# Optimization experiments

Hardware: AMD Instinct MI355X
Metric: run time of the kernel (lower is better)

Reference implementation:

```python
import jax, jax.numpy as jnp
import numpy as np
import math

IN_FEATURES = 1024
OUT_FEATURES = 1024
GRID_SIZE = 5
SPLINE_ORDER = 3
BATCH = 4096
K = GRID_SIZE + 2 * SPLINE_ORDER  # 11 basis functions per feature


def make_grid():
    h = (1.0 - (-1.0)) / GRID_SIZE
    xx = np.arange(-SPLINE_ORDER, GRID_SIZE + SPLINE_ORDER + 1, dtype=np.float32) * h + (-1.0)
    return jnp.asarray(np.broadcast_to(xx, (IN_FEATURES, xx.shape[0])).copy())  # (in, K+1)


def setup_inputs() -> dict:
    key = jax.random.key(0)
    k1, k2, k3, k4 = jax.random.split(key, 4)
    x = jax.random.normal(k1, (BATCH, IN_FEATURES), dtype=jnp.float32)
    base_weight = jax.random.normal(k2, (OUT_FEATURES, IN_FEATURES), dtype=jnp.float32) * 0.02
    spline_weight = jax.random.normal(k3, (OUT_FEATURES, IN_FEATURES, K), dtype=jnp.float32) * 0.02
    spline_scaler = jax.random.normal(k4, (OUT_FEATURES, IN_FEATURES), dtype=jnp.float32) * 0.1
    return {"x": x, "base_weight": base_weight, "spline_weight": spline_weight,
            "spline_scaler": spline_scaler, "grid": make_grid()}


def trig_basis(x, grid):
    # x: (B, in) ; grid: (in, K+1) -> basis: (B, in, K)
    a = grid[:, :-1]                      # (in, K)
    b = grid[:, 1:]                       # (in, K)
    interval = jnp.maximum(b - a, 1e-8)
    xe = x[:, :, None]                    # (B, in, 1)
    inside = ((xe >= a) & (xe < b)).astype(x.dtype)
    trig = jnp.sin(jnp.pi * (xe - a) / interval)
    return inside * trig


def reference(x, base_weight, spline_weight, spline_scaler, grid):
    # base branch: SiLU(x) @ base_weight^T
    enm = jax.nn.silu(x) @ base_weight.T                     # (B, out)
    # spline branch: fused basis expansion + GEMM
    basis = trig_basis(x, grid)                              # (B, in, K)
    sw = spline_weight * spline_scaler[:, :, None]           # (out, in, K)
    snm = jnp.einsum('bik,oik->bo', basis, sw)               # (B, out)
    return enm + snm
```

## Files before the change

### kernel.cpp

```cpp
#include <hip/hip_runtime.h>
#include <hip/hip_bf16.h>

#define BATCH  4096
#define INF    1024
#define OUTF   1024
#define KSPL   11
#define KSPB   11264
#define SW_SCALE 1016.0f

using bf16    = __hip_bfloat16;
using short8  = __attribute__((ext_vector_type(8))) short;
using ushort8 = __attribute__((ext_vector_type(8))) unsigned short;
using f32x4   = __attribute__((ext_vector_type(4))) float;
using i32x4   = __attribute__((ext_vector_type(4))) int;
typedef unsigned long long u64;

__device__ __forceinline__ unsigned short f2bf(float f){
  union { float f; unsigned u; } a; a.f = f;
  return (unsigned short)((a.u + 0x7FFFu + ((a.u >> 16) & 1u)) >> 16);
}

__device__ __forceinline__ void llds16(const void* g, const void* l){
  __builtin_amdgcn_global_load_lds(
      (const __attribute__((address_space(1))) unsigned int*)g,
      (__attribute__((address_space(3))) unsigned int*)l, 16, 0, 0);
}

__device__ __forceinline__ void bar(){
  asm volatile("" ::: "memory");
  __builtin_amdgcn_s_barrier();
  asm volatile("" ::: "memory");
}

__device__ __forceinline__ f32x4 mfma16(short8 a, short8 b, f32x4 c){
  return __builtin_amdgcn_mfma_f32_16x16x32_bf16(a, b, c, 0, 0, 0);
}
__device__ __forceinline__ i32x4 mfma_i8(i32x4 a, i32x4 b, i32x4 c){
  return __builtin_amdgcn_mfma_i32_16x16x64_i8(a, b, c, 0, 0, 0);
}

__device__ __forceinline__ int swz(int L){ return L ^ (((L>>7)&7)<<4); }

__global__ __launch_bounds__(256) void prep(const float* __restrict__ x,
                                            const float* __restrict__ bw,
                                            const float* __restrict__ sw,
                                            const float* __restrict__ sc,
                                            bf16* __restrict__ A_sil,
                                            char* __restrict__ A_spl,
                                            bf16* __restrict__ W_b,
                                            char* __restrict__ W_s){
  const int t = threadIdx.x;
  if (blockIdx.x < 2048){
    const int gid = blockIdx.x * 256 + t;
    const int b  = gid >> 7;
    const int i0 = (gid & 127) * 8;
    const float* xr = x + (size_t)b * INF + i0;
    f32x4 p0 = *(const f32x4*)xr;
    f32x4 p1 = *(const f32x4*)(xr + 4);
    float v[8];
    #pragma unroll
    for (int j = 0; j < 4; ++j){ v[j] = p0[j]; v[4+j] = p1[j]; }
    ushort8 sl;
    int c[8], q[8];
    #pragma unroll
    for (int j = 0; j < 8; ++j){
      float xx = v[j];
      sl[j] = f2bf(xx / (1.0f + __expf(-xx)));
      float tt = (xx + 1.0f) * 2.5f;
      float fl = floorf(tt);
      c[j] = (int)fl + 3;
      q[j] = (int)rintf(__sinf(3.14159265358979f * (tt - fl)) * 127.0f);
    }
    *(ushort8*)(A_sil + (size_t)b*INF + i0) = sl;
    char* ar = A_spl + (size_t)b * KSPB + i0;
    #pragma unroll
    for (int k = 0; k < KSPL; ++k){
      u64 up = 0;
      #pragma unroll
      for (int j = 0; j < 8; ++j){
        unsigned char byte = (c[j] == k) ? (unsigned char)q[j] : (unsigned char)0;
        up |= ((u64)byte) << (8*j);
      }
      *(u64*)(ar + k*INF) = up;
    }
  } else {
    const int gid = (blockIdx.x - 2048) * 256 + t;
    const int o  = gid >> 7;
    const int i0 = (gid & 127) * 8;
    float buf[88];
    const float* sp = sw + ((size_t)o*INF + i0) * KSPL;
    #pragma unroll
    for (int qd = 0; qd < 22; ++qd)
      ((f32x4*)buf)[qd] = ((const f32x4*)sp)[qd];
    f32x4 c0 = *(const f32x4*)(sc + (size_t)o*INF + i0);
    f32x4 c1 = *(const f32x4*)(sc + (size_t)o*INF + i0 + 4);
    float scv[8];
    #pragma unroll
    for (int j = 0; j < 4; ++j){ scv[j] = c0[j]; scv[4+j] = c1[j]; }
    {
      const float* br = bw + (size_t)o*INF + i0;
      f32x4 v0 = *(const f32x4*)br;
      f32x4 v1 = *(const f32x4*)(br + 4);
      ushort8 u;
      #pragma unroll
      for (int j = 0; j < 4; ++j){ u[j] = f2bf(v0[j]); u[4+j] = f2bf(v1[j]); }
      *(ushort8*)(W_b + (size_t)o*INF + i0) = u;
    }
    char* wr = W_s + (size_t)o * KSPB + i0;
    #pragma unroll
    for (int k = 0; k < KSPL; ++k){
      u64 up = 0;
      #pragma unroll
      for (int j = 0; j < 8; ++j){
        float vv = buf[j*KSPL + k] * scv[j] * SW_SCALE;
        vv = fminf(fmaxf(vv, -127.0f), 127.0f);
        int qq = (int)rintf(vv);
        up |= ((u64)(unsigned char)(signed char)qq) << (8*j);
      }
      *(u64*)(wr + k*INF) = up;
    }
  }
}

template<int NS>
__global__ __launch_bounds__(512, 2) void gemm_i8k(const char* __restrict__ A,
                                                   const char* __restrict__ W,
                                                   short* __restrict__ Cp){
  constexpr int KSPLIT_B = KSPB / NS;
  constexpr int NG       = KSPLIT_B / 64;
  __shared__ __align__(16) char smem[131072];

  const int bid = blockIdx.x;
  const int xcd = bid & 7, local = bid >> 3;
  const int split = xcd >> 1;
  const int mt    = (xcd & 1) * 8 + (local >> 2);
  const int nt    = local & 3;
  const int bm = mt*256, bn = nt*256;

  const int t    = threadIdx.x;
  const int lane = t & 63, w = t >> 6;
  const int wr = w >> 2, wc = w & 3;
  const int r15 = lane & 15, hi = lane >> 4;

  int offA[8], offB[4];
  #pragma unroll
  for (int m = 0; m < 8; ++m){
    int L = (wr*128 + m*16 + r15)*64 + hi*16;
    offA[m] = swz(L);
  }
  #pragma unroll
  for (int n = 0; n < 4; ++n){
    int L = (wc*64 + n*16 + r15)*64 + hi*16;
    offB[n] = 16384 + swz(L);
  }

  const char* gA[2]; const char* gB[2];
  int ldsA[2], ldsB[2];
  #pragma unroll
  for (int j = 0; j < 2; ++j){
    int P = (t + j*512)*16;
    int L = swz(P);
    int row = L >> 6, inner = L & 63;
    gA[j] = A + (size_t)(bm + row)*KSPB + split*KSPLIT_B + inner;
    gB[j] = W + (size_t)(bn + row)*KSPB + split*KSPLIT_B + inner;
    ldsA[j] = j*8192 + w*1024;
    ldsB[j] = 16384 + j*8192 + w*1024;
  }

  #define STAGE(buf, tile) do{ \
    llds16(gA[0] + (tile)*64, smem + (buf)*32768 + ldsA[0]); \
    llds16(gA[1] + (tile)*64, smem + (buf)*32768 + ldsA[1]); \
    llds16(gB[0] + (tile)*64, smem + (buf)*32768 + ldsB[0]); \
    llds16(gB[1] + (tile)*64, smem + (buf)*32768 + ldsB[1]); }while(0)

  i32x4 acc[8][4] = {};
  i32x4 afA[4], afB[4], bfA[4], bfB[4];

  STAGE(0,0);
  STAGE(1,1);
  asm volatile("s_waitcnt vmcnt(4)" ::: "memory");
  bar();
  #pragma unroll
  for (int n = 0; n < 4; ++n) bfA[n] = *(const i32x4*)(smem + offB[n]);
  #pragma unroll
  for (int m = 0; m < 4; ++m) afA[m] = *(const i32x4*)(smem + offA[m]);

  #define BODY(tt, curA, curB, nxtA, nxtB) do{                                \
    const char* bp_ = smem + ((tt)&3)*32768;                                  \
    const char* bq_ = smem + (((tt)+1)&3)*32768;                              \
    if ((tt) + 2 < NG){                                                       \
      STAGE(((tt)+2)&3, (tt)+2);                                              \
      asm volatile("s_waitcnt vmcnt(4)" ::: "memory");                        \
    } else {                                                                  \
      asm volatile("s_waitcnt vmcnt(0)" ::: "memory");                        \
    }                                                                         \
    bar();                                                                    \
    i32x4 ag_[4];                                                             \
    __builtin_amdgcn_s_setprio(1);                                            \
    _Pragma("unroll")                                                         \
    for (int m = 0; m < 4; ++m){                                              \
      ag_[m] = *(const i32x4*)(bp_ + offA[4+m]);                              \
      _Pragma("unroll")                                                       \
      for (int n = 0; n < 4; ++n)                                             \
        acc[m][n] = mfma_i8(curA[m], curB[n], acc[m][n]);                     \
    }                                                                         \
    _Pragma("unroll")                                                         \
    for (int m = 0; m < 4; ++m){                                              \
      if ((tt) + 1 < NG){                                                     \
        nxtA[m] = *(const i32x4*)(bq_ + offA[m]);                             \
        nxtB[m] = *(const i32x4*)(bq_ + offB[m]);                             \
      }                                                                       \
      _Pragma("unroll")                                                       \
      for (int n = 0; n < 4; ++n)                                             \
        acc[4+m][n] = mfma_i8(ag_[m], curB[n], acc[4+m][n]);                  \
    }                                                                         \
    __builtin_amdgcn_s_setprio(0);                                            \
  }while(0)

  #pragma unroll 1
  for (int s = 0; s < NG/2; ++s){
    BODY(2*s,   afA, bfA, afB, bfB);
    BODY(2*s+1, afB, bfB, afA, bfA);
  }
  #undef BODY
  #undef STAGE

  short* outp = Cp + (size_t)split * (BATCH*OUTF);
  #pragma unroll
  for (int m = 0; m < 8; ++m){
    const int r0 = bm + wr*128 + m*16 + hi*4;
    #pragma unroll
    for (int n = 0; n < 4; ++n){
      const int cc = bn + wc*64 + n*16 + r15;
      #pragma unroll
      for (int j = 0; j < 4; ++j){
        int v = acc[m][n][j];
        v = (v >  32767) ?  32767 : v;
        v = (v < -32768) ? -32768 : v;
        outp[(size_t)(r0 + j) * OUTF + cc] = (short)v;
      }
    }
  }
}

__global__ __launch_bounds__(512, 2) void gemm_e(const bf16* __restrict__ A,
                                                 const bf16* __restrict__ W,
                                                 const short* __restrict__ Cp,
                                                 float* __restrict__ out){
  constexpr int NG = 32;
  __shared__ __align__(16) char smem[49152];

  const int bid = blockIdx.x;
  const int fin = (bid & 7) * 32 + (bid >> 3);
  const int mt = fin >> 3, nt = fin & 7;
  const int bm = mt*128, bn = nt*128;

  const int t    = threadIdx.x;
  const int lane = t & 63, w = t >> 6;
  const int wr = w >> 2, wc = w & 3;
  const int r15 = lane & 15, hi = lane >> 4;

  int offA[4], offB[2];
  #pragma unroll
  for (int m = 0; m < 4; ++m){
    int L = (wr*64 + m*16 + r15)*64 + hi*16;
    offA[m] = swz(L);
  }
  #pragma unroll
  for (int n = 0; n < 2; ++n){
    int L = (wc*32 + n*16 + r15)*64 + hi*16;
    offB[n] = 8192 + swz(L);
  }

  const char* gA; const char* gB;
  {
    int P = t*16;
    int L = swz(P);
    int row = L >> 6, inner = L & 63;
    gA = (const char*)A + (size_t)(bm + row)*2048 + inner;
    gB = (const char*)W + (size_t)(bn + row)*2048 + inner;
  }
  const int ldsA = w*1024;
  const int ldsB = 8192 + w*1024;

  #define STAGE(buf, tile) do{ \
    llds16(gA + (tile)*64, smem + (buf)*16384 + ldsA); \
    llds16(gB + (tile)*64, smem + (buf)*16384 + ldsB); }while(0)

  f32x4 acc[4][2] = {};
  short8 afA[4], afB[4], bfA[2], bfB[2];

  STAGE(0,0);
  STAGE(1,1);
  asm volatile("s_waitcnt vmcnt(2)" ::: "memory");
  bar();
  #pragma unroll
  for (int m = 0; m < 4; ++m) afA[m] = *(const short8*)(smem + offA[m]);
  #pragma unroll
  for (int n = 0; n < 2; ++n) bfA[n] = *(const short8*)(smem + offB[n]);

  #define BODY(tt, curA, curB, nxtA, nxtB) do{                                \
    int nb_ = ((tt)+1) % 3;                                                   \
    const char* bq_ = smem + nb_*16384;                                       \
    if ((tt) + 2 < NG){                                                       \
      STAGE(((tt)+2) % 3, (tt)+2);                                            \
      asm volatile("s_waitcnt vmcnt(2)" ::: "memory");                        \
    } else {                                                                  \
      asm volatile("s_waitcnt vmcnt(0)" ::: "memory");                        \
    }                                                                         \
    bar();                                                                    \
    __builtin_amdgcn_s_setprio(1);                                            \
    _Pragma("unroll")                                                         \
    for (int m = 0; m < 4; ++m){                                              \
      if ((tt) + 1 < NG){                                                     \
        nxtA[m] = *(const short8*)(bq_ + offA[m]);                            \
        if (m < 2) nxtB[m] = *(const short8*)(bq_ + offB[m]);                 \
      }                                                                       \
      _Pragma("unroll")                                                       \
      for (int n = 0; n < 2; ++n)                                             \
        acc[m][n] = mfma16(curA[m], curB[n], acc[m][n]);                      \
    }                                                                         \
    __builtin_amdgcn_s_setprio(0);                                            \
  }while(0)

  #pragma unroll 1
  for (int s = 0; s < NG/2; ++s){
    BODY(2*s,   afA, bfA, afB, bfB);
    BODY(2*s+1, afB, bfB, afA, bfA);
  }
  #undef BODY
  #undef STAGE

  const float invP = 1.0f / (127.0f * SW_SCALE);
  const size_t NN = (size_t)BATCH * OUTF;
  #pragma unroll
  for (int m = 0; m < 4; ++m){
    const int r0 = bm + wr*64 + m*16 + hi*4;
    #pragma unroll
    for (int n = 0; n < 2; ++n){
      const int cc = bn + wc*32 + n*16 + r15;
      #pragma unroll
      for (int j = 0; j < 4; ++j){
        const size_t idx = (size_t)(r0 + j) * OUTF + cc;
        int s4 = (int)Cp[idx] + (int)Cp[NN + idx]
               + (int)Cp[2*NN + idx] + (int)Cp[3*NN + idx];
        out[idx] = acc[m][n][j] + (float)s4 * invP;
      }
    }
  }
}

__global__ __launch_bounds__(256) void fallback(const float* __restrict__ x,
    const float* __restrict__ bw, const float* __restrict__ sw,
    const float* __restrict__ sc, float* __restrict__ out){
  const int b = blockIdx.x, t = threadIdx.x;
  __shared__ float ls[INF], sg[INF];
  __shared__ int   lc[INF];
  for (int i = t; i < INF; i += 256){
    float xx = x[(size_t)b*INF + i];
    ls[i] = xx / (1.0f + __expf(-xx));
    float tt = (xx + 1.0f)*2.5f;
    float fl = floorf(tt);
    int c = (int)fl + 3;
    lc[i] = ((unsigned)c < 11u) ? c : -1;
    sg[i] = __sinf(3.14159265358979f*(tt - fl));
  }
  __syncthreads();
  for (int o = t; o < OUTF; o += 256){
    float acc = 0.f;
    const float* bwr = bw + (size_t)o*INF;
    const float* swr = sw + (size_t)o*INF*KSPL;
    const float* scr = sc + (size_t)o*INF;
    for (int i = 0; i < INF; ++i){
      acc = fmaf(ls[i], bwr[i], acc);
      int c = lc[i];
      if (c >= 0) acc = fmaf(sg[i]*scr[i], swr[i*KSPL + c], acc);
    }
    out[(size_t)b*OUTF + o] = acc;
  }
}

extern "C" void kernel_launch(void* const* d_in, const int* in_sizes, int n_in,
                              void* d_out, int out_size, void* d_ws, size_t ws_size,
                              hipStream_t stream){
  const float* x  = (const float*)d_in[0];
  const float* bw = (const float*)d_in[1];
  const float* sw = (const float*)d_in[2];
  const float* sc = (const float*)d_in[3];
  float* out = (float*)d_out;
  const size_t oAsil = 0;
  const size_t oAspl = oAsil + (size_t)BATCH*INF*2;
  const size_t oWb   = oAspl + (size_t)BATCH*KSPB;
  const size_t oWs   = oWb   + (size_t)OUTF*INF*2;
  const size_t oCp   = oWs   + (size_t)OUTF*KSPB;
  const size_t total = oCp   + (size_t)4*BATCH*OUTF*2;
  if (ws_size >= total){
    bf16*  A_sil = (bf16*)((char*)d_ws + oAsil);
    char*  A_spl = (char*)d_ws + oAspl;
    bf16*  W_b   = (bf16*)((char*)d_ws + oWb);
    char*  W_s   = (char*)d_ws + oWs;
    short* Cp    = (short*)((char*)d_ws + oCp);
    hipLaunchKernelGGL(prep, dim3(2560), dim3(256), 0, stream,
                       x, bw, sw, sc, A_sil, A_spl, W_b, W_s);
    gemm_i8k<4><<<dim3(256), dim3(512), 0, stream>>>(A_spl, W_s, Cp);
    gemm_e<<<dim3(256), dim3(512), 0, stream>>>(A_sil, W_b, Cp, out);
  } else {
    hipLaunchKernelGGL(fallback, dim3(BATCH), dim3(256), 0, stream, x, bw, sw, sc, out);
  }
}
```

Measured before the change: 95.17 us.

## Simplify int8 spline GEMM to double-buffered LDS with smaller shared memory

Replaces the 4-stage LDS ring with register-level fragment prefetch by a plain 2-stage double buffer. Each tile now loads its fragments after the barrier and adds a trailing barrier. LDS drops from 128KB to 64KB and launch bounds ask for 4 blocks per CU. The goal is more resident waves to hide latency, but the kernel gives up the cross-tile prefetch and adds an extra barrier per tile. The 256-block grid may not fill the extra occupancy.

```diff
diff --git a/kernel.cpp b/kernel.cpp
--- a/kernel.cpp
+++ b/kernel.cpp
@@ -123,12 +123,12 @@
 }
 
 template<int NS>
-__global__ __launch_bounds__(512, 2) void gemm_i8k(const char* __restrict__ A,
+__global__ __launch_bounds__(512, 4) void gemm_i8c(const char* __restrict__ A,
                                                    const char* __restrict__ W,
                                                    short* __restrict__ Cp){
   constexpr int KSPLIT_B = KSPB / NS;
   constexpr int NG       = KSPLIT_B / 64;
-  __shared__ __align__(16) char smem[131072];
+  __shared__ __align__(16) char smem[65536];
 
   const int bid = blockIdx.x;
   const int xcd = bid & 7, local = bid >> 3;
@@ -174,55 +174,40 @@
     llds16(gB[1] + (tile)*64, smem + (buf)*32768 + ldsB[1]); }while(0)
 
   i32x4 acc[8][4] = {};
-  i32x4 afA[4], afB[4], bfA[4], bfB[4];
 
   STAGE(0,0);
-  STAGE(1,1);
-  asm volatile("s_waitcnt vmcnt(4)" ::: "memory");
-  bar();
-  #pragma unroll
-  for (int n = 0; n < 4; ++n) bfA[n] = *(const i32x4*)(smem + offB[n]);
-  #pragma unroll
-  for (int m = 0; m < 4; ++m) afA[m] = *(const i32x4*)(smem + offA[m]);
-
-  #define BODY(tt, curA, curB, nxtA, nxtB) do{                                \
-    const char* bp_ = smem + ((tt)&3)*32768;                                  \
-    const char* bq_ = smem + (((tt)+1)&3)*32768;                              \
-    if ((tt) + 2 < NG){                                                       \
-      STAGE(((tt)+2)&3, (tt)+2);                                              \
-      asm volatile("s_waitcnt vmcnt(4)" ::: "memory");                        \
-    } else {                                                                  \
-      asm volatile("s_waitcnt vmcnt(0)" ::: "memory");                        \
-    }                                                                         \
-    bar();                                                                    \
-    i32x4 ag_[4];                                                             \
-    __builtin_amdgcn_s_setprio(1);                                            \
-    _Pragma("unroll")                                                         \
-    for (int m = 0; m < 4; ++m){                                              \
-      ag_[m] = *(const i32x4*)(bp_ + offA[4+m]);                              \
-      _Pragma("unroll")                                                       \
-      for (int n = 0; n < 4; ++n)                                             \
-        acc[m][n] = mfma_i8(curA[m], curB[n], acc[m][n]);                     \
-    }                                                                         \
-    _Pragma("unroll")                                                         \
-    for (int m = 0; m < 4; ++m){                                              \
-      if ((tt) + 1 < NG){                                                     \
-        nxtA[m] = *(const i32x4*)(bq_ + offA[m]);                             \
-        nxtB[m] = *(const i32x4*)(bq_ + offB[m]);                             \
-      }                                                                       \
-      _Pragma("unroll")                                                       \
-      for (int n = 0; n < 4; ++n)                                             \
-        acc[4+m][n] = mfma_i8(ag_[m], curB[n], acc[4+m][n]);                  \
-    }                                                                         \
-    __builtin_amdgcn_s_setprio(0);                                            \
-  }while(0)
 
   #pragma unroll 1
-  for (int s = 0; s < NG/2; ++s){
-    BODY(2*s,   afA, bfA, afB, bfB);
-    BODY(2*s+1, afB, bfB, afA, bfA);
-  }
-  #undef BODY
+  for (int tt = 0; tt < NG; ++tt){
+    if (tt + 1 < NG){
+      STAGE((tt+1)&1, tt+1);
+      asm volatile("s_waitcnt vmcnt(4)" ::: "memory");
+    } else {
+      asm volatile("s_waitcnt vmcnt(0)" ::: "memory");
+    }
+    bar();
+    const char* bp = smem + (tt&1)*32768;
+    i32x4 af[4], ag[4], bf[4];
+    #pragma unroll
+    for (int m = 0; m < 4; ++m) af[m] = *(const i32x4*)(bp + offA[m]);
+    #pragma unroll
+    for (int n = 0; n < 4; ++n) bf[n] = *(const i32x4*)(bp + offB[n]);
+    __builtin_amdgcn_s_setprio(1);
+    #pragma unroll
+    for (int m = 0; m < 4; ++m){
+      ag[m] = *(const i32x4*)(bp + offA[4+m]);
+      #pragma unroll
+      for (int n = 0; n < 4; ++n)
+        acc[m][n] = mfma_i8(af[m], bf[n], acc[m][n]);
+    }
+    #pragma unroll
+    for (int m = 0; m < 4; ++m)
+      #pragma unroll
+      for (int n = 0; n < 4; ++n)
+        acc[4+m][n] = mfma_i8(ag[m], bf[n], acc[4+m][n]);
+    __builtin_amdgcn_s_setprio(0);
+    bar();
+  }
   #undef STAGE
 
   short* outp = Cp + (size_t)split * (BATCH*OUTF);
@@ -402,7 +387,7 @@
     short* Cp    = (short*)((char*)d_ws + oCp);
     hipLaunchKernelGGL(prep, dim3(2560), dim3(256), 0, stream,
                        x, bw, sw, sc, A_sil, A_spl, W_b, W_s);
-    gemm_i8k<4><<<dim3(256), dim3(512), 0, stream>>>(A_spl, W_s, Cp);
+    gemm_i8c<4><<<dim3(256), dim3(512), 0, stream>>>(A_spl, W_s, Cp);
     gemm_e<<<dim3(256), dim3(512), 0, stream>>>(A_sil, W_b, Cp, out);
   } else {
     hipLaunchKernelGGL(fallback, dim3(BATCH), dim3(256), 0, stream, x, bw, sw, sc, out);
```

Measured after the change: 377.6 us. 3.97x slower.
